# Kernel optimization log

Measured on AMD Instinct MI355X. Metric: run time of the kernel, lower is better.

Reference implementation:

```python
import jax, jax.numpy as jnp
import numpy as np

N_HEAD = 16

def _rope(t, cos, sin):
    # t: [B,T,H,hd]; cos/sin: [T, hd//2]
    B, T, H, hd = t.shape
    tr = t.reshape(B, T, H, hd // 2, 2)
    t0, t1 = tr[..., 0], tr[..., 1]
    c = cos[None, :T, None, :]
    s = sin[None, :T, None, :]
    out = jnp.stack([t0 * c - t1 * s, t0 * s + t1 * c], axis=-1)
    return out.reshape(B, T, H, hd)

def setup_inputs() -> dict:
    key = jax.random.key(0)
    B, T, D = 2, 2048, 1024
    hd = D // N_HEAD
    ks = jax.random.split(key, 5)
    x = jax.random.normal(ks[0], (B, T, D), dtype=jnp.float32)
    Wq = jax.random.normal(ks[1], (D, D), dtype=jnp.float32) * 0.02
    Wk = jax.random.normal(ks[2], (D, D), dtype=jnp.float32) * 0.02
    Wv = jax.random.normal(ks[3], (D, D), dtype=jnp.float32) * 0.02
    Wo = jax.random.normal(ks[4], (D, D), dtype=jnp.float32) * 0.02
    # Real rotary tables (cos/sin of theta-based angles), matching precompute_freqs_cis
    theta = 10000.0
    inv_freq = 1.0 / (theta ** (np.arange(0, hd, 2, dtype=np.float32) / hd))
    ang = np.outer(np.arange(T, dtype=np.float32), inv_freq)  # [T, hd//2]
    freqs_cos = jnp.asarray(np.cos(ang), dtype=jnp.float32)
    freqs_sin = jnp.asarray(np.sin(ang), dtype=jnp.float32)
    return {"x": x, "Wq": Wq, "Wk": Wk, "Wv": Wv, "Wo": Wo,
            "freqs_cos": freqs_cos, "freqs_sin": freqs_sin}

def reference(x, Wq, Wk, Wv, Wo, freqs_cos, freqs_sin):
    B, T, D = x.shape
    H = N_HEAD
    hd = D // H
    scale = hd ** -0.5
    q = (x @ Wq.T).reshape(B, T, H, hd)
    k = (x @ Wk.T).reshape(B, T, H, hd)
    v = (x @ Wv.T).reshape(B, T, H, hd)
    q = _rope(q, freqs_cos, freqs_sin)
    k = _rope(k, freqs_cos, freqs_sin)
    # scores: [B,H,T,T]
    scores = jnp.einsum('bqhd,bkhd->bhqk', q, k) * scale
    causal = jnp.tril(jnp.ones((T, T), dtype=bool))
    scores = jnp.where(causal[None, None], scores, -jnp.inf)
    attn = jax.nn.softmax(scores, axis=-1)
    out = jnp.einsum('bhqk,bkhd->bqhd', attn, v).reshape(B, T, D)
    return out @ Wo.T
```

## Files before the change

### kernel.cpp

```cpp
#include <hip/hip_runtime.h>
#include <math.h>

typedef __bf16 bf16;
typedef __bf16 bf16x8 __attribute__((ext_vector_type(8)));
typedef __bf16 bf16x4 __attribute__((ext_vector_type(4)));
typedef __bf16 bf16x2 __attribute__((ext_vector_type(2)));
typedef float  f32x4  __attribute__((ext_vector_type(4)));

#define B_DIM 2
#define T_LEN 2048
#define D_DIM 1024
#define N_HEAD 16
#define HEAD_D 64
#define M_ROWS (B_DIM * T_LEN)

#define GLDS16(g, l)                                                          \
    __builtin_amdgcn_global_load_lds(                                         \
        (const __attribute__((address_space(1))) void*)(g),                   \
        (__attribute__((address_space(3))) void*)(l), 16, 0, 0)

__global__ void prep_cvt(const float* __restrict__ x, const float* __restrict__ wq,
                         const float* __restrict__ wk, const float* __restrict__ wv,
                         const float* __restrict__ wo, bf16* __restrict__ xb,
                         bf16* __restrict__ wqkv, bf16* __restrict__ wob) {
    int id = blockIdx.x * blockDim.x + threadIdx.x;
    if (id >= (1 << 21)) return;
    const float* src; bf16* dst; int off;
    if (id < (1 << 20)) { src = x; dst = xb; off = id; }
    else {
        int r = id - (1 << 20);
        int wi = r >> 18;
        off = r & ((1 << 18) - 1);
        src = wi == 0 ? wq : wi == 1 ? wk : wi == 2 ? wv : wo;
        dst = wi < 3 ? wqkv + ((size_t)wi << 20) : wob;
    }
    float4 v = reinterpret_cast<const float4*>(src)[off];
    bf16x4 w;
    w[0] = (bf16)v.x; w[1] = (bf16)v.y; w[2] = (bf16)v.z; w[3] = (bf16)v.w;
    reinterpret_cast<bf16x4*>(dst)[off] = w;
}

template <int MODE>
__global__ __launch_bounds__(256)
void gemm_glds(const bf16* __restrict__ A, const bf16* __restrict__ Bm,
               bf16* __restrict__ q, bf16* __restrict__ k, bf16* __restrict__ v,
               float* __restrict__ outf) {
    constexpr int K = D_DIM;
    __shared__ bf16 As[128 * 64];
    __shared__ bf16 Bs[128 * 64];
    const int tid = threadIdx.x, lane = tid & 63, wave = tid >> 6;
    const int wr = wave >> 1, wc = wave & 1;
    const int rowg = lane >> 4, col0 = lane & 15;

    const int nwg = gridDim.x * gridDim.y, cpx = nwg >> 3;
    const int lin = blockIdx.x + blockIdx.y * gridDim.x;
    const int nid = (lin & 7) * cpx + (lin >> 3);
    const int bx = nid % gridDim.x, by = nid / gridDim.x;
    const int m0 = by * 128, n0 = bx * 128;

    const int srow = lane >> 3;
    const int schk = (lane & 7) ^ srow;
    const bf16* gA = A + (size_t)(m0 + wave * 32 + srow) * K + schk * 8;
    const bf16* gB = Bm + (size_t)(n0 + wave * 32 + srow) * K + schk * 8;

    f32x4 acc[4][4];
    f32x4 zero = {0.f, 0.f, 0.f, 0.f};
#pragma unroll
    for (int i = 0; i < 4; i++)
#pragma unroll
        for (int j = 0; j < 4; j++) acc[i][j] = zero;

    for (int k0 = 0; k0 < K; k0 += 64) {
#pragma unroll
        for (int t = 0; t < 4; ++t) {
            GLDS16(gA + k0 + t * 8 * K, &As[(wave * 32 + t * 8) * 64]);
            GLDS16(gB + k0 + t * 8 * K, &Bs[(wave * 32 + t * 8) * 64]);
        }
        __syncthreads();
#pragma unroll
        for (int kk = 0; kk < 2; ++kk) {
            bf16x8 af[4], bfr[4];
#pragma unroll
            for (int i = 0; i < 4; i++) {
                int R = wr * 64 + i * 16 + col0;
                af[i] = *reinterpret_cast<const bf16x8*>(&As[R * 64 + (((kk * 4 + rowg) ^ (R & 7)) * 8)]);
            }
#pragma unroll
            for (int j = 0; j < 4; j++) {
                int R = wc * 64 + j * 16 + col0;
                bfr[j] = *reinterpret_cast<const bf16x8*>(&Bs[R * 64 + (((kk * 4 + rowg) ^ (R & 7)) * 8)]);
            }
#pragma unroll
            for (int i = 0; i < 4; i++)
#pragma unroll
                for (int j = 0; j < 4; j++)
                    acc[i][j] = __builtin_amdgcn_mfma_f32_16x16x32_bf16(af[i], bfr[j], acc[i][j], 0, 0, 0);
        }
        __syncthreads();
    }

    if constexpr (MODE == 0) {
        const int which = bx >> 3;
        if (which < 2) {
            bf16* dst = which == 0 ? q : k;
#pragma unroll
            for (int i = 0; i < 4; i++)
#pragma unroll
                for (int j = 0; j < 4; j++)
#pragma unroll
                    for (int r = 0; r < 4; r++) {
                        int m = m0 + wr * 64 + i * 16 + rowg * 4 + r;
                        int n = (n0 + wc * 64 + j * 16 + col0) & 1023;
                        int b = m >> 11, t = m & 2047, h = n >> 6, d = n & 63;
                        dst[(((size_t)(b * N_HEAD + h)) * T_LEN + t) * HEAD_D + d] = (bf16)acc[i][j][r];
                    }
        } else {
#pragma unroll
            for (int i = 0; i < 4; i++)
#pragma unroll
                for (int j = 0; j < 4; j++) {
                    bf16x4 pk;
#pragma unroll
                    for (int r = 0; r < 4; r++) pk[r] = (bf16)acc[i][j][r];
                    int m = m0 + wr * 64 + i * 16 + rowg * 4;
                    int n = (n0 + wc * 64 + j * 16 + col0) & 1023;
                    int b = m >> 11, t = m & 2047, h = n >> 6, d = n & 63;
                    *reinterpret_cast<bf16x4*>(
                        &v[(((size_t)(b * N_HEAD + h)) * HEAD_D + d) * T_LEN + t]) = pk;
                }
        }
    } else {
#pragma unroll
        for (int i = 0; i < 4; i++)
#pragma unroll
            for (int j = 0; j < 4; j++)
#pragma unroll
                for (int r = 0; r < 4; r++) {
                    int m = m0 + wr * 64 + i * 16 + rowg * 4 + r;
                    int n = n0 + wc * 64 + j * 16 + col0;
                    outf[(size_t)m * D_DIM + n] = acc[i][j][r];
                }
    }
}

__global__ void rope_inplace(bf16* __restrict__ q, bf16* __restrict__ k,
                             const float* __restrict__ cosT, const float* __restrict__ sinT) {
    int id = blockIdx.x * blockDim.x + threadIdx.x;
    int i = id & 31;
    int t = (id >> 5) & 2047;
    int bh = id >> 16;
    float c = cosT[t * 32 + i], s = sinT[t * 32 + i];
    size_t p = ((size_t)bh * T_LEN + t) * HEAD_D + 2 * i;
    float q0 = (float)q[p], q1 = (float)q[p + 1];
    q[p]     = (bf16)((q0 * c - q1 * s) * 0.125f);
    q[p + 1] = (bf16)((q0 * s + q1 * c) * 0.125f);
    float k0 = (float)k[p], k1 = (float)k[p + 1];
    k[p]     = (bf16)(k0 * c - k1 * s);
    k[p + 1] = (bf16)(k0 * s + k1 * c);
}

__global__ __launch_bounds__(512)
void attn_fwd(const bf16* __restrict__ qh, const bf16* __restrict__ kh,
              const bf16* __restrict__ vtg, bf16* __restrict__ ao) {
    __shared__ __align__(16) bf16 Ks[2][64 * 64];
    __shared__ __align__(16) bf16 Vs[2][64 * 64];
    __shared__ __align__(16) bf16 Ps[8][16][72];
    const int tid = threadIdx.x, lane = tid & 63, w = tid >> 6;
    const int g = lane >> 4, q15 = lane & 15;
    const int lin = blockIdx.x + blockIdx.y * 8;
    const int nid = (lin & 7) * 32 + (lin >> 3);
    const int pi = nid & 7, bh = nid >> 3;
    const size_t kbase = (size_t)bh * T_LEN * HEAD_D;
    const size_t vbase = (size_t)bh * HEAD_D * T_LEN;
    const int srow = tid >> 3, scg = tid & 7;
    const int sel = srow * 64 + ((scg * 8) ^ ((srow & 7) * 8));
    const int ksw = (q15 & 7) * 8;

    const float NEGINF = -__builtin_inff();
    f32x4 zero = {0.f, 0.f, 0.f, 0.f};

    for (int ph = 0; ph < 2; ++ph) {
        const int qi = ph ? (15 - pi) : pi;
        const int q0 = qi * 128;
        const int nt = 2 * qi + 2;
        const int qlo = q0 + w * 16;

        bf16x8 aq[2];
#pragma unroll
        for (int kk = 0; kk < 2; ++kk)
            aq[kk] = *reinterpret_cast<const bf16x8*>(
                &qh[kbase + (size_t)(qlo + q15) * HEAD_D + kk * 32 + g * 8]);

        f32x4 o[4];
#pragma unroll
        for (int j = 0; j < 4; j++) o[j] = zero;
        float mi = NEGINF, li = 0.f;

        {
            uint4 kr = *reinterpret_cast<const uint4*>(&kh[kbase + (size_t)srow * HEAD_D + scg * 8]);
            uint4 vr = *reinterpret_cast<const uint4*>(&vtg[vbase + (size_t)srow * T_LEN + scg * 8]);
            *reinterpret_cast<uint4*>(&Ks[0][sel]) = kr;
            *reinterpret_cast<uint4*>(&Vs[0][sel]) = vr;
        }
        __syncthreads();

        for (int kt = 0; kt < nt; ++kt) {
            const int cur = kt & 1;
            const int kv0 = kt * 64;
            const bool pf = (kt + 1 < nt);
            uint4 kr, vr;
            if (pf) {
                kr = *reinterpret_cast<const uint4*>(&kh[kbase + (size_t)(kv0 + 64 + srow) * HEAD_D + scg * 8]);
                vr = *reinterpret_cast<const uint4*>(&vtg[vbase + (size_t)srow * T_LEN + kv0 + 64 + scg * 8]);
            }

            f32x4 sT[4];
#pragma unroll
            for (int j = 0; j < 4; j++) sT[j] = zero;
            __builtin_amdgcn_s_setprio(1);
#pragma unroll
            for (int kk = 0; kk < 2; ++kk) {
                const int ko = (kk * 32 + g * 8) ^ ksw;
#pragma unroll
                for (int j = 0; j < 4; j++) {
                    bf16x8 bk = *reinterpret_cast<const bf16x8*>(&Ks[cur][(j * 16 + q15) * 64 + ko]);
                    sT[j] = __builtin_amdgcn_mfma_f32_16x16x32_bf16(bk, aq[kk], sT[j], 0, 0, 0);
                }
            }
            __builtin_amdgcn_s_setprio(0);
            if (kv0 + 63 > qlo) {
                const int qg = qlo + q15;
#pragma unroll
                for (int j = 0; j < 4; j++)
#pragma unroll
                    for (int r = 0; r < 4; r++)
                        if (kv0 + j * 16 + g * 4 + r > qg) sT[j][r] = NEGINF;
            }
            float mx = sT[0][0];
#pragma unroll
            for (int j = 0; j < 4; j++)
#pragma unroll
                for (int r = 0; r < 4; r++) mx = fmaxf(mx, sT[j][r]);
            mx = fmaxf(mx, __shfl_xor(mx, 16));
            mx = fmaxf(mx, __shfl_xor(mx, 32));
            const float mnew = fmaxf(mi, mx);
            const float al = __expf(mi - mnew);
            float ps = 0.f;
#pragma unroll
            for (int j = 0; j < 4; j++)
#pragma unroll
                for (int r = 0; r < 4; r++) {
                    float p = __expf(sT[j][r] - mnew);
                    sT[j][r] = p;
                    ps += p;
                }
            ps += __shfl_xor(ps, 16);
            ps += __shfl_xor(ps, 32);
            li = li * al + ps;
            mi = mnew;
#pragma unroll
            for (int j = 0; j < 4; j++)
#pragma unroll
                for (int pr = 0; pr < 2; ++pr) {
                    bf16x2 pk;
                    pk[0] = (bf16)sT[j][2 * pr];
                    pk[1] = (bf16)sT[j][2 * pr + 1];
                    *reinterpret_cast<bf16x2*>(&Ps[w][q15][j * 16 + g * 4 + 2 * pr]) = pk;
                }
#pragma unroll
            for (int j = 0; j < 4; j++)
#pragma unroll
                for (int r = 0; r < 4; r++) o[j][r] *= al;
            __builtin_amdgcn_s_setprio(1);
#pragma unroll
            for (int kk = 0; kk < 2; ++kk) {
                bf16x8 pb = *reinterpret_cast<const bf16x8*>(&Ps[w][q15][kk * 32 + g * 8]);
                const int ko = (kk * 32 + g * 8) ^ ksw;
#pragma unroll
                for (int j = 0; j < 4; j++) {
                    bf16x8 av = *reinterpret_cast<const bf16x8*>(&Vs[cur][(j * 16 + q15) * 64 + ko]);
                    o[j] = __builtin_amdgcn_mfma_f32_16x16x32_bf16(av, pb, o[j], 0, 0, 0);
                }
            }
            __builtin_amdgcn_s_setprio(0);
            if (pf) {
                *reinterpret_cast<uint4*>(&Ks[cur ^ 1][sel]) = kr;
                *reinterpret_cast<uint4*>(&Vs[cur ^ 1][sel]) = vr;
            }
            __syncthreads();
        }

        const int b = bh >> 4, h = bh & 15;
        const float inv = 1.f / li;
        const int t = qlo + q15;
        bf16* dst = &ao[((size_t)(b * T_LEN + t)) * D_DIM + h * HEAD_D];
#pragma unroll
        for (int j = 0; j < 4; j++) {
            bf16x4 pk;
#pragma unroll
            for (int r = 0; r < 4; r++) pk[r] = (bf16)(o[j][r] * inv);
            *reinterpret_cast<bf16x4*>(&dst[j * 16 + g * 4]) = pk;
        }
    }
}

extern "C" void kernel_launch(void* const* d_in, const int* in_sizes, int n_in,
                              void* d_out, int out_size, void* d_ws, size_t ws_size,
                              hipStream_t stream) {
    const float* x  = (const float*)d_in[0];
    const float* Wq = (const float*)d_in[1];
    const float* Wk = (const float*)d_in[2];
    const float* Wv = (const float*)d_in[3];
    const float* Wo = (const float*)d_in[4];
    const float* fc = (const float*)d_in[5];
    const float* fs = (const float*)d_in[6];
    float* out = (float*)d_out;

    char* ws = (char*)d_ws;
    const size_t MB = 1024 * 1024;
    bf16* xb   = (bf16*)(ws);
    bf16* wqkv = (bf16*)(ws + 8 * MB);
    bf16* wob  = (bf16*)(ws + 14 * MB);
    bf16* qhd  = (bf16*)(ws + 16 * MB);
    bf16* khd  = (bf16*)(ws + 24 * MB);
    bf16* vt   = (bf16*)(ws + 32 * MB);
    bf16* ao   = (bf16*)(ws + 40 * MB);

    prep_cvt<<<8192, 256, 0, stream>>>(x, Wq, Wk, Wv, Wo, xb, wqkv, wob);

    dim3 gq(24, 32);
    gemm_glds<0><<<gq, 256, 0, stream>>>(xb, wqkv, qhd, khd, vt, nullptr);

    rope_inplace<<<(B_DIM * N_HEAD * T_LEN * 32) / 256, 256, 0, stream>>>(qhd, khd, fc, fs);

    dim3 ga(8, B_DIM * N_HEAD);
    attn_fwd<<<ga, 512, 0, stream>>>(qhd, khd, vt, ao);

    dim3 go(8, 32);
    gemm_glds<1><<<go, 256, 0, stream>>>(ao, wob, nullptr, nullptr, nullptr, out);
}
```

Measured before the change: 119.8 us.

## Double-buffer GEMM LDS staging and split attention into one q-tile per block

```diff
diff --git a/kernel.cpp b/kernel.cpp
--- a/kernel.cpp
+++ b/kernel.cpp
@@ -41,13 +41,13 @@
 }
 
 template <int MODE>
-__global__ __launch_bounds__(256)
+__global__ __launch_bounds__(256, 2)
 void gemm_glds(const bf16* __restrict__ A, const bf16* __restrict__ Bm,
                bf16* __restrict__ q, bf16* __restrict__ k, bf16* __restrict__ v,
                float* __restrict__ outf) {
     constexpr int K = D_DIM;
-    __shared__ bf16 As[128 * 64];
-    __shared__ bf16 Bs[128 * 64];
+    __shared__ bf16 As[2][128 * 64];
+    __shared__ bf16 Bs[2][128 * 64];
     const int tid = threadIdx.x, lane = tid & 63, wave = tid >> 6;
     const int wr = wave >> 1, wc = wave & 1;
     const int rowg = lane >> 4, col0 = lane & 15;
@@ -70,34 +70,55 @@
 #pragma unroll
         for (int j = 0; j < 4; j++) acc[i][j] = zero;
 
-    for (int k0 = 0; k0 < K; k0 += 64) {
+    auto stage = [&](int kt, int buf) {
+        const int koff = kt * 64;
 #pragma unroll
         for (int t = 0; t < 4; ++t) {
-            GLDS16(gA + k0 + t * 8 * K, &As[(wave * 32 + t * 8) * 64]);
-            GLDS16(gB + k0 + t * 8 * K, &Bs[(wave * 32 + t * 8) * 64]);
-        }
-        __syncthreads();
+            GLDS16(gA + koff + t * 8 * K, &As[buf][(wave * 32 + t * 8) * 64]);
+            GLDS16(gB + koff + t * 8 * K, &Bs[buf][(wave * 32 + t * 8) * 64]);
+        }
+    };
+    auto compute_tile = [&](int cur) {
 #pragma unroll
         for (int kk = 0; kk < 2; ++kk) {
             bf16x8 af[4], bfr[4];
 #pragma unroll
             for (int i = 0; i < 4; i++) {
                 int R = wr * 64 + i * 16 + col0;
-                af[i] = *reinterpret_cast<const bf16x8*>(&As[R * 64 + (((kk * 4 + rowg) ^ (R & 7)) * 8)]);
+                af[i] = *reinterpret_cast<const bf16x8*>(&As[cur][R * 64 + (((kk * 4 + rowg) ^ (R & 7)) * 8)]);
             }
 #pragma unroll
             for (int j = 0; j < 4; j++) {
                 int R = wc * 64 + j * 16 + col0;
-                bfr[j] = *reinterpret_cast<const bf16x8*>(&Bs[R * 64 + (((kk * 4 + rowg) ^ (R & 7)) * 8)]);
-            }
+                bfr[j] = *reinterpret_cast<const bf16x8*>(&Bs[cur][R * 64 + (((kk * 4 + rowg) ^ (R & 7)) * 8)]);
+            }
+            __builtin_amdgcn_s_setprio(1);
 #pragma unroll
             for (int i = 0; i < 4; i++)
 #pragma unroll
                 for (int j = 0; j < 4; j++)
                     acc[i][j] = __builtin_amdgcn_mfma_f32_16x16x32_bf16(af[i], bfr[j], acc[i][j], 0, 0, 0);
-        }
-        __syncthreads();
-    }
+            __builtin_amdgcn_s_setprio(0);
+        }
+    };
+
+    stage(0, 0);
+    stage(1, 1);
+#pragma unroll 1
+    for (int kt = 0; kt < 15; ++kt) {
+        const int cur = kt & 1;
+        asm volatile("s_waitcnt vmcnt(8)" ::: "memory");
+        __builtin_amdgcn_s_barrier();
+        __builtin_amdgcn_sched_barrier(0);
+        compute_tile(cur);
+        __builtin_amdgcn_sched_barrier(0);
+        __builtin_amdgcn_s_barrier();
+        __builtin_amdgcn_sched_barrier(0);
+        if (kt < 14) stage(kt + 2, cur);
+    }
+    asm volatile("s_waitcnt vmcnt(0)" ::: "memory");
+    __builtin_amdgcn_s_barrier();
+    compute_tile(1);
 
     if constexpr (MODE == 0) {
         const int which = bx >> 3;
@@ -159,7 +180,7 @@
     k[p + 1] = (bf16)(k0 * s + k1 * c);
 }
 
-__global__ __launch_bounds__(512)
+__global__ __launch_bounds__(512, 4)
 void attn_fwd(const bf16* __restrict__ qh, const bf16* __restrict__ kh,
               const bf16* __restrict__ vtg, bf16* __restrict__ ao) {
     __shared__ __align__(16) bf16 Ks[2][64 * 64];
@@ -167,9 +188,9 @@
     __shared__ __align__(16) bf16 Ps[8][16][72];
     const int tid = threadIdx.x, lane = tid & 63, w = tid >> 6;
     const int g = lane >> 4, q15 = lane & 15;
-    const int lin = blockIdx.x + blockIdx.y * 8;
-    const int nid = (lin & 7) * 32 + (lin >> 3);
-    const int pi = nid & 7, bh = nid >> 3;
+    const int lin = blockIdx.x + blockIdx.y * 16;
+    const int nid = (lin & 7) * 64 + (lin >> 3);
+    const int bh = nid >> 4, qi = 15 - (nid & 15);
     const size_t kbase = (size_t)bh * T_LEN * HEAD_D;
     const size_t vbase = (size_t)bh * HEAD_D * T_LEN;
     const int srow = tid >> 3, scg = tid & 7;
@@ -179,128 +200,125 @@
     const float NEGINF = -__builtin_inff();
     f32x4 zero = {0.f, 0.f, 0.f, 0.f};
 
-    for (int ph = 0; ph < 2; ++ph) {
-        const int qi = ph ? (15 - pi) : pi;
-        const int q0 = qi * 128;
-        const int nt = 2 * qi + 2;
-        const int qlo = q0 + w * 16;
-
-        bf16x8 aq[2];
-#pragma unroll
-        for (int kk = 0; kk < 2; ++kk)
-            aq[kk] = *reinterpret_cast<const bf16x8*>(
-                &qh[kbase + (size_t)(qlo + q15) * HEAD_D + kk * 32 + g * 8]);
-
-        f32x4 o[4];
-#pragma unroll
-        for (int j = 0; j < 4; j++) o[j] = zero;
-        float mi = NEGINF, li = 0.f;
-
-        {
-            uint4 kr = *reinterpret_cast<const uint4*>(&kh[kbase + (size_t)srow * HEAD_D + scg * 8]);
-            uint4 vr = *reinterpret_cast<const uint4*>(&vtg[vbase + (size_t)srow * T_LEN + scg * 8]);
-            *reinterpret_cast<uint4*>(&Ks[0][sel]) = kr;
-            *reinterpret_cast<uint4*>(&Vs[0][sel]) = vr;
+    const int q0 = qi * 128;
+    const int nt = 2 * qi + 2;
+    const int qlo = q0 + w * 16;
+
+    bf16x8 aq[2];
+#pragma unroll
+    for (int kk = 0; kk < 2; ++kk)
+        aq[kk] = *reinterpret_cast<const bf16x8*>(
+            &qh[kbase + (size_t)(qlo + q15) * HEAD_D + kk * 32 + g * 8]);
+
+    f32x4 o[4];
+#pragma unroll
+    for (int j = 0; j < 4; j++) o[j] = zero;
+    float mi = NEGINF, li = 0.f;
+
+    {
+        uint4 kr = *reinterpret_cast<const uint4*>(&kh[kbase + (size_t)srow * HEAD_D + scg * 8]);
+        uint4 vr = *reinterpret_cast<const uint4*>(&vtg[vbase + (size_t)srow * T_LEN + scg * 8]);
+        *reinterpret_cast<uint4*>(&Ks[0][sel]) = kr;
+        *reinterpret_cast<uint4*>(&Vs[0][sel]) = vr;
+    }
+    __syncthreads();
+
+    for (int kt = 0; kt < nt; ++kt) {
+        const int cur = kt & 1;
+        const int kv0 = kt * 64;
+        const bool pf = (kt + 1 < nt);
+        uint4 kr, vr;
+        if (pf) {
+            kr = *reinterpret_cast<const uint4*>(&kh[kbase + (size_t)(kv0 + 64 + srow) * HEAD_D + scg * 8]);
+            vr = *reinterpret_cast<const uint4*>(&vtg[vbase + (size_t)srow * T_LEN + kv0 + 64 + scg * 8]);
+        }
+
+        f32x4 sT[4];
+#pragma unroll
+        for (int j = 0; j < 4; j++) sT[j] = zero;
+        __builtin_amdgcn_s_setprio(1);
+#pragma unroll
+        for (int kk = 0; kk < 2; ++kk) {
+            const int ko = (kk * 32 + g * 8) ^ ksw;
+#pragma unroll
+            for (int j = 0; j < 4; j++) {
+                bf16x8 bk = *reinterpret_cast<const bf16x8*>(&Ks[cur][(j * 16 + q15) * 64 + ko]);
+                sT[j] = __builtin_amdgcn_mfma_f32_16x16x32_bf16(bk, aq[kk], sT[j], 0, 0, 0);
+            }
+        }
+        __builtin_amdgcn_s_setprio(0);
+        if (kv0 + 63 > qlo) {
+            const int qg = qlo + q15;
+#pragma unroll
+            for (int j = 0; j < 4; j++)
+#pragma unroll
+                for (int r = 0; r < 4; r++)
+                    if (kv0 + j * 16 + g * 4 + r > qg) sT[j][r] = NEGINF;
+        }
+        float mx = sT[0][0];
+#pragma unroll
+        for (int j = 0; j < 4; j++)
+#pragma unroll
+            for (int r = 0; r < 4; r++) mx = fmaxf(mx, sT[j][r]);
+        mx = fmaxf(mx, __shfl_xor(mx, 16));
+        mx = fmaxf(mx, __shfl_xor(mx, 32));
+        const float mnew = fmaxf(mi, mx);
+        const float al = __expf(mi - mnew);
+        float ps = 0.f;
+#pragma unroll
+        for (int j = 0; j < 4; j++)
+#pragma unroll
+            for (int r = 0; r < 4; r++) {
+                float p = __expf(sT[j][r] - mnew);
+                sT[j][r] = p;
+                ps += p;
+            }
+        ps += __shfl_xor(ps, 16);
+        ps += __shfl_xor(ps, 32);
+        li = li * al + ps;
+        mi = mnew;
+#pragma unroll
+        for (int j = 0; j < 4; j++)
+#pragma unroll
+            for (int pr = 0; pr < 2; ++pr) {
+                bf16x2 pk;
+                pk[0] = (bf16)sT[j][2 * pr];
+                pk[1] = (bf16)sT[j][2 * pr + 1];
+                *reinterpret_cast<bf16x2*>(&Ps[w][q15][j * 16 + g * 4 + 2 * pr]) = pk;
+            }
+#pragma unroll
+        for (int j = 0; j < 4; j++)
+#pragma unroll
+            for (int r = 0; r < 4; r++) o[j][r] *= al;
+        __builtin_amdgcn_s_setprio(1);
+#pragma unroll
+        for (int kk = 0; kk < 2; ++kk) {
+            bf16x8 pb = *reinterpret_cast<const bf16x8*>(&Ps[w][q15][kk * 32 + g * 8]);
+            const int ko = (kk * 32 + g * 8) ^ ksw;
+#pragma unroll
+            for (int j = 0; j < 4; j++) {
+                bf16x8 av = *reinterpret_cast<const bf16x8*>(&Vs[cur][(j * 16 + q15) * 64 + ko]);
+                o[j] = __builtin_amdgcn_mfma_f32_16x16x32_bf16(av, pb, o[j], 0, 0, 0);
+            }
+        }
+        __builtin_amdgcn_s_setprio(0);
+        if (pf) {
+            *reinterpret_cast<uint4*>(&Ks[cur ^ 1][sel]) = kr;
+            *reinterpret_cast<uint4*>(&Vs[cur ^ 1][sel]) = vr;
         }
         __syncthreads();
-
-        for (int kt = 0; kt < nt; ++kt) {
-            const int cur = kt & 1;
-            const int kv0 = kt * 64;
-            const bool pf = (kt + 1 < nt);
-            uint4 kr, vr;
-            if (pf) {
-                kr = *reinterpret_cast<const uint4*>(&kh[kbase + (size_t)(kv0 + 64 + srow) * HEAD_D + scg * 8]);
-                vr = *reinterpret_cast<const uint4*>(&vtg[vbase + (size_t)srow * T_LEN + kv0 + 64 + scg * 8]);
-            }
-
-            f32x4 sT[4];
-#pragma unroll
-            for (int j = 0; j < 4; j++) sT[j] = zero;
-            __builtin_amdgcn_s_setprio(1);
-#pragma unroll
-            for (int kk = 0; kk < 2; ++kk) {
-                const int ko = (kk * 32 + g * 8) ^ ksw;
-#pragma unroll
-                for (int j = 0; j < 4; j++) {
-                    bf16x8 bk = *reinterpret_cast<const bf16x8*>(&Ks[cur][(j * 16 + q15) * 64 + ko]);
-                    sT[j] = __builtin_amdgcn_mfma_f32_16x16x32_bf16(bk, aq[kk], sT[j], 0, 0, 0);
-                }
-            }
-            __builtin_amdgcn_s_setprio(0);
-            if (kv0 + 63 > qlo) {
-                const int qg = qlo + q15;
-#pragma unroll
-                for (int j = 0; j < 4; j++)
-#pragma unroll
-                    for (int r = 0; r < 4; r++)
-                        if (kv0 + j * 16 + g * 4 + r > qg) sT[j][r] = NEGINF;
-            }
-            float mx = sT[0][0];
-#pragma unroll
-            for (int j = 0; j < 4; j++)
-#pragma unroll
-                for (int r = 0; r < 4; r++) mx = fmaxf(mx, sT[j][r]);
-            mx = fmaxf(mx, __shfl_xor(mx, 16));
-            mx = fmaxf(mx, __shfl_xor(mx, 32));
-            const float mnew = fmaxf(mi, mx);
-            const float al = __expf(mi - mnew);
-            float ps = 0.f;
-#pragma unroll
-            for (int j = 0; j < 4; j++)
-#pragma unroll
-                for (int r = 0; r < 4; r++) {
-                    float p = __expf(sT[j][r] - mnew);
-                    sT[j][r] = p;
-                    ps += p;
-                }
-            ps += __shfl_xor(ps, 16);
-            ps += __shfl_xor(ps, 32);
-            li = li * al + ps;
-            mi = mnew;
-#pragma unroll
-            for (int j = 0; j < 4; j++)
-#pragma unroll
-                for (int pr = 0; pr < 2; ++pr) {
-                    bf16x2 pk;
-                    pk[0] = (bf16)sT[j][2 * pr];
-                    pk[1] = (bf16)sT[j][2 * pr + 1];
-                    *reinterpret_cast<bf16x2*>(&Ps[w][q15][j * 16 + g * 4 + 2 * pr]) = pk;
-                }
-#pragma unroll
-            for (int j = 0; j < 4; j++)
-#pragma unroll
-                for (int r = 0; r < 4; r++) o[j][r] *= al;
-            __builtin_amdgcn_s_setprio(1);
-#pragma unroll
-            for (int kk = 0; kk < 2; ++kk) {
-                bf16x8 pb = *reinterpret_cast<const bf16x8*>(&Ps[w][q15][kk * 32 + g * 8]);
-                const int ko = (kk * 32 + g * 8) ^ ksw;
-#pragma unroll
-                for (int j = 0; j < 4; j++) {
-                    bf16x8 av = *reinterpret_cast<const bf16x8*>(&Vs[cur][(j * 16 + q15) * 64 + ko]);
-                    o[j] = __builtin_amdgcn_mfma_f32_16x16x32_bf16(av, pb, o[j], 0, 0, 0);
-                }
-            }
-            __builtin_amdgcn_s_setprio(0);
-            if (pf) {
-                *reinterpret_cast<uint4*>(&Ks[cur ^ 1][sel]) = kr;
-                *reinterpret_cast<uint4*>(&Vs[cur ^ 1][sel]) = vr;
-            }
-            __syncthreads();
-        }
-
-        const int b = bh >> 4, h = bh & 15;
-        const float inv = 1.f / li;
-        const int t = qlo + q15;
-        bf16* dst = &ao[((size_t)(b * T_LEN + t)) * D_DIM + h * HEAD_D];
-#pragma unroll
-        for (int j = 0; j < 4; j++) {
-            bf16x4 pk;
-#pragma unroll
-            for (int r = 0; r < 4; r++) pk[r] = (bf16)(o[j][r] * inv);
-            *reinterpret_cast<bf16x4*>(&dst[j * 16 + g * 4]) = pk;
-        }
+    }
+
+    const int b = bh >> 4, h = bh & 15;
+    const float inv = 1.f / li;
+    const int t = qlo + q15;
+    bf16* dst = &ao[((size_t)(b * T_LEN + t)) * D_DIM + h * HEAD_D];
+#pragma unroll
+    for (int j = 0; j < 4; j++) {
+        bf16x4 pk;
+#pragma unroll
+        for (int r = 0; r < 4; r++) pk[r] = (bf16)(o[j][r] * inv);
+        *reinterpret_cast<bf16x4*>(&dst[j * 16 + g * 4]) = pk;
     }
 }
 
@@ -333,7 +351,7 @@
 
     rope_inplace<<<(B_DIM * N_HEAD * T_LEN * 32) / 256, 256, 0, stream>>>(qhd, khd, fc, fs);
 
-    dim3 ga(8, B_DIM * N_HEAD);
+    dim3 ga(16, B_DIM * N_HEAD);
     attn_fwd<<<ga, 512, 0, stream>>>(qhd, khd, vt, ao);
 
     dim3 go(8, 32);
```

New measurement: 130.5 us. 1.09x slower.

## Fuse Q rope into attention and retile attention to 64-row query blocks

Applied to the files above, without the earlier changes.

```diff
diff --git a/kernel.cpp b/kernel.cpp
--- a/kernel.cpp
+++ b/kernel.cpp
@@ -41,7 +41,7 @@
 }
 
 template <int MODE>
-__global__ __launch_bounds__(256)
+__global__ __launch_bounds__(256, 4)
 void gemm_glds(const bf16* __restrict__ A, const bf16* __restrict__ Bm,
                bf16* __restrict__ q, bf16* __restrict__ k, bf16* __restrict__ v,
                float* __restrict__ outf) {
@@ -70,7 +70,9 @@
 #pragma unroll
         for (int j = 0; j < 4; j++) acc[i][j] = zero;
 
-    for (int k0 = 0; k0 < K; k0 += 64) {
+#pragma unroll 1
+    for (int kt = 0; kt < 16; ++kt) {
+        const int k0 = kt * 64;
 #pragma unroll
         for (int t = 0; t < 4; ++t) {
             GLDS16(gA + k0 + t * 8 * K, &As[(wave * 32 + t * 8) * 64]);
@@ -143,164 +145,185 @@
     }
 }
 
-__global__ void rope_inplace(bf16* __restrict__ q, bf16* __restrict__ k,
-                             const float* __restrict__ cosT, const float* __restrict__ sinT) {
+__global__ void rope_k(bf16* __restrict__ k, const float* __restrict__ cosT,
+                       const float* __restrict__ sinT) {
     int id = blockIdx.x * blockDim.x + threadIdx.x;
     int i = id & 31;
     int t = (id >> 5) & 2047;
     int bh = id >> 16;
     float c = cosT[t * 32 + i], s = sinT[t * 32 + i];
     size_t p = ((size_t)bh * T_LEN + t) * HEAD_D + 2 * i;
-    float q0 = (float)q[p], q1 = (float)q[p + 1];
-    q[p]     = (bf16)((q0 * c - q1 * s) * 0.125f);
-    q[p + 1] = (bf16)((q0 * s + q1 * c) * 0.125f);
     float k0 = (float)k[p], k1 = (float)k[p + 1];
     k[p]     = (bf16)(k0 * c - k1 * s);
     k[p + 1] = (bf16)(k0 * s + k1 * c);
 }
 
-__global__ __launch_bounds__(512)
+__device__ inline bf16x8 rope8(bf16x8 v, f32x4 c4, f32x4 s4, float scale) {
+    bf16x8 r;
+#pragma unroll
+    for (int m = 0; m < 4; ++m) {
+        float a = (float)v[2 * m], b = (float)v[2 * m + 1];
+        r[2 * m]     = (bf16)((a * c4[m] - b * s4[m]) * scale);
+        r[2 * m + 1] = (bf16)((a * s4[m] + b * c4[m]) * scale);
+    }
+    return r;
+}
+
+__global__ __launch_bounds__(256, 3)
 void attn_fwd(const bf16* __restrict__ qh, const bf16* __restrict__ kh,
-              const bf16* __restrict__ vtg, bf16* __restrict__ ao) {
+              const bf16* __restrict__ vtg, const float* __restrict__ fc,
+              const float* __restrict__ fs, bf16* __restrict__ ao) {
     __shared__ __align__(16) bf16 Ks[2][64 * 64];
     __shared__ __align__(16) bf16 Vs[2][64 * 64];
-    __shared__ __align__(16) bf16 Ps[8][16][72];
+    __shared__ __align__(16) bf16 Ps[4][16][72];
     const int tid = threadIdx.x, lane = tid & 63, w = tid >> 6;
     const int g = lane >> 4, q15 = lane & 15;
-    const int lin = blockIdx.x + blockIdx.y * 8;
-    const int nid = (lin & 7) * 32 + (lin >> 3);
-    const int pi = nid & 7, bh = nid >> 3;
+    const int lin = blockIdx.x;
+    const int xcd = lin & 7, idx = lin >> 3;
+    const int qi = 31 - (idx >> 2);
+    const int bh = xcd * 4 + (idx & 3);
     const size_t kbase = (size_t)bh * T_LEN * HEAD_D;
     const size_t vbase = (size_t)bh * HEAD_D * T_LEN;
-    const int srow = tid >> 3, scg = tid & 7;
-    const int sel = srow * 64 + ((scg * 8) ^ ((srow & 7) * 8));
+    const int c0row = tid >> 3, ccg = tid & 7;
+    const int swz = (ccg * 8) ^ ((c0row & 7) * 8);
+    const int sel0 = c0row * 64 + swz;
+    const int sel1 = sel0 + 32 * 64;
     const int ksw = (q15 & 7) * 8;
 
     const float NEGINF = -__builtin_inff();
     f32x4 zero = {0.f, 0.f, 0.f, 0.f};
 
-    for (int ph = 0; ph < 2; ++ph) {
-        const int qi = ph ? (15 - pi) : pi;
-        const int q0 = qi * 128;
-        const int nt = 2 * qi + 2;
-        const int qlo = q0 + w * 16;
-
-        bf16x8 aq[2];
-#pragma unroll
-        for (int kk = 0; kk < 2; ++kk)
-            aq[kk] = *reinterpret_cast<const bf16x8*>(
-                &qh[kbase + (size_t)(qlo + q15) * HEAD_D + kk * 32 + g * 8]);
-
-        f32x4 o[4];
-#pragma unroll
-        for (int j = 0; j < 4; j++) o[j] = zero;
-        float mi = NEGINF, li = 0.f;
-
-        {
-            uint4 kr = *reinterpret_cast<const uint4*>(&kh[kbase + (size_t)srow * HEAD_D + scg * 8]);
-            uint4 vr = *reinterpret_cast<const uint4*>(&vtg[vbase + (size_t)srow * T_LEN + scg * 8]);
-            *reinterpret_cast<uint4*>(&Ks[0][sel]) = kr;
-            *reinterpret_cast<uint4*>(&Vs[0][sel]) = vr;
+    const int nt = qi + 1;
+    const int qlo = qi * 64 + w * 16;
+
+    bf16x8 aq[2];
+#pragma unroll
+    for (int kk = 0; kk < 2; ++kk) {
+        bf16x8 qv = *reinterpret_cast<const bf16x8*>(
+            &qh[kbase + (size_t)(qlo + q15) * HEAD_D + kk * 32 + g * 8]);
+        f32x4 c4 = *reinterpret_cast<const f32x4*>(&fc[(qlo + q15) * 32 + kk * 16 + g * 4]);
+        f32x4 s4 = *reinterpret_cast<const f32x4*>(&fs[(qlo + q15) * 32 + kk * 16 + g * 4]);
+        aq[kk] = rope8(qv, c4, s4, 0.125f);
+    }
+
+    f32x4 o[4];
+#pragma unroll
+    for (int j = 0; j < 4; j++) o[j] = zero;
+    float mi = NEGINF, li = 0.f;
+
+    {
+        uint4 k0a = *reinterpret_cast<const uint4*>(&kh[kbase + (size_t)c0row * HEAD_D + ccg * 8]);
+        uint4 k0b = *reinterpret_cast<const uint4*>(&kh[kbase + (size_t)(c0row + 32) * HEAD_D + ccg * 8]);
+        uint4 v0a = *reinterpret_cast<const uint4*>(&vtg[vbase + (size_t)c0row * T_LEN + ccg * 8]);
+        uint4 v0b = *reinterpret_cast<const uint4*>(&vtg[vbase + (size_t)(c0row + 32) * T_LEN + ccg * 8]);
+        *reinterpret_cast<uint4*>(&Ks[0][sel0]) = k0a;
+        *reinterpret_cast<uint4*>(&Ks[0][sel1]) = k0b;
+        *reinterpret_cast<uint4*>(&Vs[0][sel0]) = v0a;
+        *reinterpret_cast<uint4*>(&Vs[0][sel1]) = v0b;
+    }
+    __syncthreads();
+
+    for (int kt = 0; kt < nt; ++kt) {
+        const int cur = kt & 1;
+        const int kv0 = kt * 64;
+        const bool pf = (kt + 1 < nt);
+        uint4 kra, krb, vra, vrb;
+        if (pf) {
+            const int kn = kv0 + 64;
+            kra = *reinterpret_cast<const uint4*>(&kh[kbase + (size_t)(kn + c0row) * HEAD_D + ccg * 8]);
+            krb = *reinterpret_cast<const uint4*>(&kh[kbase + (size_t)(kn + c0row + 32) * HEAD_D + ccg * 8]);
+            vra = *reinterpret_cast<const uint4*>(&vtg[vbase + (size_t)c0row * T_LEN + kn + ccg * 8]);
+            vrb = *reinterpret_cast<const uint4*>(&vtg[vbase + (size_t)(c0row + 32) * T_LEN + kn + ccg * 8]);
+        }
+
+        f32x4 sT[4];
+#pragma unroll
+        for (int j = 0; j < 4; j++) sT[j] = zero;
+        __builtin_amdgcn_s_setprio(1);
+#pragma unroll
+        for (int kk = 0; kk < 2; ++kk) {
+            const int ko = (kk * 32 + g * 8) ^ ksw;
+#pragma unroll
+            for (int j = 0; j < 4; j++) {
+                bf16x8 bk = *reinterpret_cast<const bf16x8*>(&Ks[cur][(j * 16 + q15) * 64 + ko]);
+                sT[j] = __builtin_amdgcn_mfma_f32_16x16x32_bf16(bk, aq[kk], sT[j], 0, 0, 0);
+            }
+        }
+        __builtin_amdgcn_s_setprio(0);
+        if (kv0 + 63 > qlo) {
+            const int qg = qlo + q15;
+#pragma unroll
+            for (int j = 0; j < 4; j++)
+#pragma unroll
+                for (int r = 0; r < 4; r++)
+                    if (kv0 + j * 16 + g * 4 + r > qg) sT[j][r] = NEGINF;
+        }
+        float mx = sT[0][0];
+#pragma unroll
+        for (int j = 0; j < 4; j++)
+#pragma unroll
+            for (int r = 0; r < 4; r++) mx = fmaxf(mx, sT[j][r]);
+        mx = fmaxf(mx, __shfl_xor(mx, 16));
+        mx = fmaxf(mx, __shfl_xor(mx, 32));
+        const float mnew = fmaxf(mi, mx);
+        const float al = __expf(mi - mnew);
+        float ps = 0.f;
+#pragma unroll
+        for (int j = 0; j < 4; j++)
+#pragma unroll
+            for (int r = 0; r < 4; r++) {
+                float p = __expf(sT[j][r] - mnew);
+                sT[j][r] = p;
+                ps += p;
+            }
+        ps += __shfl_xor(ps, 16);
+        ps += __shfl_xor(ps, 32);
+        li = li * al + ps;
+        mi = mnew;
+#pragma unroll
+        for (int j = 0; j < 4; j++)
+#pragma unroll
+            for (int pr = 0; pr < 2; ++pr) {
+                bf16x2 pk;
+                pk[0] = (bf16)sT[j][2 * pr];
+                pk[1] = (bf16)sT[j][2 * pr + 1];
+                *reinterpret_cast<bf16x2*>(&Ps[w][q15][j * 16 + g * 4 + 2 * pr]) = pk;
+            }
+#pragma unroll
+        for (int j = 0; j < 4; j++)
+#pragma unroll
+            for (int r = 0; r < 4; r++) o[j][r] *= al;
+        __builtin_amdgcn_s_setprio(1);
+#pragma unroll
+        for (int kk = 0; kk < 2; ++kk) {
+            bf16x8 pb = *reinterpret_cast<const bf16x8*>(&Ps[w][q15][kk * 32 + g * 8]);
+            const int ko = (kk * 32 + g * 8) ^ ksw;
+#pragma unroll
+            for (int j = 0; j < 4; j++) {
+                bf16x8 av = *reinterpret_cast<const bf16x8*>(&Vs[cur][(j * 16 + q15) * 64 + ko]);
+                o[j] = __builtin_amdgcn_mfma_f32_16x16x32_bf16(av, pb, o[j], 0, 0, 0);
+            }
+        }
+        __builtin_amdgcn_s_setprio(0);
+        if (pf) {
+            *reinterpret_cast<uint4*>(&Ks[cur ^ 1][sel0]) = kra;
+            *reinterpret_cast<uint4*>(&Ks[cur ^ 1][sel1]) = krb;
+            *reinterpret_cast<uint4*>(&Vs[cur ^ 1][sel0]) = vra;
+            *reinterpret_cast<uint4*>(&Vs[cur ^ 1][sel1]) = vrb;
         }
         __syncthreads();
-
-        for (int kt = 0; kt < nt; ++kt) {
-            const int cur = kt & 1;
-            const int kv0 = kt * 64;
-            const bool pf = (kt + 1 < nt);
-            uint4 kr, vr;
-            if (pf) {
-                kr = *reinterpret_cast<const uint4*>(&kh[kbase + (size_t)(kv0 + 64 + srow) * HEAD_D + scg * 8]);
-                vr = *reinterpret_cast<const uint4*>(&vtg[vbase + (size_t)srow * T_LEN + kv0 + 64 + scg * 8]);
-            }
-
-            f32x4 sT[4];
-#pragma unroll
-            for (int j = 0; j < 4; j++) sT[j] = zero;
-            __builtin_amdgcn_s_setprio(1);
-#pragma unroll
-            for (int kk = 0; kk < 2; ++kk) {
-                const int ko = (kk * 32 + g * 8) ^ ksw;
-#pragma unroll
-                for (int j = 0; j < 4; j++) {
-                    bf16x8 bk = *reinterpret_cast<const bf16x8*>(&Ks[cur][(j * 16 + q15) * 64 + ko]);
-                    sT[j] = __builtin_amdgcn_mfma_f32_16x16x32_bf16(bk, aq[kk], sT[j], 0, 0, 0);
-                }
-            }
-            __builtin_amdgcn_s_setprio(0);
-            if (kv0 + 63 > qlo) {
-                const int qg = qlo + q15;
-#pragma unroll
-                for (int j = 0; j < 4; j++)
-#pragma unroll
-                    for (int r = 0; r < 4; r++)
-                        if (kv0 + j * 16 + g * 4 + r > qg) sT[j][r] = NEGINF;
-            }
-            float mx = sT[0][0];
-#pragma unroll
-            for (int j = 0; j < 4; j++)
-#pragma unroll
-                for (int r = 0; r < 4; r++) mx = fmaxf(mx, sT[j][r]);
-            mx = fmaxf(mx, __shfl_xor(mx, 16));
-            mx = fmaxf(mx, __shfl_xor(mx, 32));
-            const float mnew = fmaxf(mi, mx);
-            const float al = __expf(mi - mnew);
-            float ps = 0.f;
-#pragma unroll
-            for (int j = 0; j < 4; j++)
-#pragma unroll
-                for (int r = 0; r < 4; r++) {
-                    float p = __expf(sT[j][r] - mnew);
-                    sT[j][r] = p;
-                    ps += p;
-                }
-            ps += __shfl_xor(ps, 16);
-            ps += __shfl_xor(ps, 32);
-            li = li * al + ps;
-            mi = mnew;
-#pragma unroll
-            for (int j = 0; j < 4; j++)
-#pragma unroll
-                for (int pr = 0; pr < 2; ++pr) {
-                    bf16x2 pk;
-                    pk[0] = (bf16)sT[j][2 * pr];
-                    pk[1] = (bf16)sT[j][2 * pr + 1];
-                    *reinterpret_cast<bf16x2*>(&Ps[w][q15][j * 16 + g * 4 + 2 * pr]) = pk;
-                }
-#pragma unroll
-            for (int j = 0; j < 4; j++)
-#pragma unroll
-                for (int r = 0; r < 4; r++) o[j][r] *= al;
-            __builtin_amdgcn_s_setprio(1);
-#pragma unroll
-            for (int kk = 0; kk < 2; ++kk) {
-                bf16x8 pb = *reinterpret_cast<const bf16x8*>(&Ps[w][q15][kk * 32 + g * 8]);
-                const int ko = (kk * 32 + g * 8) ^ ksw;
-#pragma unroll
-                for (int j = 0; j < 4; j++) {
-                    bf16x8 av = *reinterpret_cast<const bf16x8*>(&Vs[cur][(j * 16 + q15) * 64 + ko]);
-                    o[j] = __builtin_amdgcn_mfma_f32_16x16x32_bf16(av, pb, o[j], 0, 0, 0);
-                }
-            }
-            __builtin_amdgcn_s_setprio(0);
-            if (pf) {
-                *reinterpret_cast<uint4*>(&Ks[cur ^ 1][sel]) = kr;
-                *reinterpret_cast<uint4*>(&Vs[cur ^ 1][sel]) = vr;
-            }
-            __syncthreads();
-        }
-
-        const int b = bh >> 4, h = bh & 15;
-        const float inv = 1.f / li;
-        const int t = qlo + q15;
-        bf16* dst = &ao[((size_t)(b * T_LEN + t)) * D_DIM + h * HEAD_D];
-#pragma unroll
-        for (int j = 0; j < 4; j++) {
-            bf16x4 pk;
-#pragma unroll
-            for (int r = 0; r < 4; r++) pk[r] = (bf16)(o[j][r] * inv);
-            *reinterpret_cast<bf16x4*>(&dst[j * 16 + g * 4]) = pk;
-        }
+    }
+
+    const int b = bh >> 4, h = bh & 15;
+    const float inv = 1.f / li;
+    const int t = qlo + q15;
+    bf16* dst = &ao[((size_t)(b * T_LEN + t)) * D_DIM + h * HEAD_D];
+#pragma unroll
+    for (int j = 0; j < 4; j++) {
+        bf16x4 pk;
+#pragma unroll
+        for (int r = 0; r < 4; r++) pk[r] = (bf16)(o[j][r] * inv);
+        *reinterpret_cast<bf16x4*>(&dst[j * 16 + g * 4]) = pk;
     }
 }
 
@@ -331,10 +354,9 @@
     dim3 gq(24, 32);
     gemm_glds<0><<<gq, 256, 0, stream>>>(xb, wqkv, qhd, khd, vt, nullptr);
 
-    rope_inplace<<<(B_DIM * N_HEAD * T_LEN * 32) / 256, 256, 0, stream>>>(qhd, khd, fc, fs);
-
-    dim3 ga(8, B_DIM * N_HEAD);
-    attn_fwd<<<ga, 512, 0, stream>>>(qhd, khd, vt, ao);
+    rope_k<<<8192, 256, 0, stream>>>(khd, fc, fs);
+
+    attn_fwd<<<1024, 256, 0, stream>>>(qhd, khd, vt, fc, fs, ao);
 
     dim3 go(8, 32);
     gemm_glds<1><<<go, 256, 0, stream>>>(ao, wob, nullptr, nullptr, nullptr, out);
```

Result: faster. 107.2 us (-10.5%).
